# Kernel tuning notes

Hardware: AMD Instinct MI355X
Metric: run time of the kernel (lower is better)

The kernel has to match this reference:

```python
import jax, jax.numpy as jnp
import numpy as np

N, F_DIM, H, K, T = 4096, 256, 256, 3, 5
START, END = 10, 3  # args.len_numerical_features, args.num_class


def setup_inputs() -> dict:
    key = jax.random.key(0)
    ks = jax.random.split(key, 8)
    s = 0.05
    x = jax.random.normal(ks[0], (N, F_DIM), dtype=jnp.float32)
    adj = jax.random.randint(ks[1], (N, N, K), 0, 2, dtype=jnp.int32)
    gnn_w = jax.random.normal(ks[2], (K, F_DIM, H), dtype=jnp.float32) * s
    gnn_b = jnp.zeros((K, H), dtype=jnp.float32)
    w_ih = jax.random.normal(ks[3], (K, 4 * H, H), dtype=jnp.float32) * s
    w_hh = jax.random.normal(ks[4], (K, 4 * H, H), dtype=jnp.float32) * s
    b_ih = jnp.zeros((K, 4 * H), dtype=jnp.float32)
    b_hh = jnp.zeros((K, 4 * H), dtype=jnp.float32)
    fc_w = jax.random.normal(ks[5], (K, F_DIM, H), dtype=jnp.float32) * s
    fc_b = jnp.zeros((K, F_DIM), dtype=jnp.float32)
    return dict(x=x, gnn_w=gnn_w, gnn_b=gnn_b, w_ih=w_ih, w_hh=w_hh,
                b_ih=b_ih, b_hh=b_hh, fc_w=fc_w, fc_b=fc_b, adj=adj)


def _gcn(x, a_bin, w, b):
    # PyG GCNConv: A_hat = A + I (self-loops added on top of existing edges,
    # weight 1), out = D^-1/2 A_hat D^-1/2 (x @ W) + b
    a = a_bin + jnp.eye(N, dtype=x.dtype)
    deg = a.sum(axis=1)
    dinv = jnp.where(deg > 0, jax.lax.rsqrt(deg), 0.0)
    a_norm = dinv[:, None] * a * dinv[None, :]
    return a_norm @ (x @ w) + b


def _lstm_last(xt, w_ih, w_hh, b_ih, b_hh):
    # batch_first LSTM over T identical inputs xt [N,H]; returns h at last step
    def step(carry, _):
        h, c = carry
        g = xt @ w_ih.T + b_ih + h @ w_hh.T + b_hh
        i, f, gg, o = jnp.split(g, 4, axis=-1)  # torch gate order: i, f, g, o
        c = jax.nn.sigmoid(f) * c + jax.nn.sigmoid(i) * jnp.tanh(gg)
        h = jax.nn.sigmoid(o) * jnp.tanh(c)
        return (h, c), None
    zero = jnp.zeros((xt.shape[0], H), dtype=xt.dtype)
    (h, c), _ = jax.lax.scan(step, (zero, zero), None, length=T)
    return h


def _sig_slice(z):
    return z.at[:, START:F_DIM - END].set(jax.nn.sigmoid(z[:, START:F_DIM - END]))


def reference(x, gnn_w, gnn_b, w_ih, w_hh, b_ih, b_hh, fc_w, fc_b, adj):
    deltas, zbars = [], []
    for k in range(K):
        a_bin = (adj[:, :, k] != 0).astype(x.dtype)
        # GCN output is identical across timesteps -> compute once
        gnn_out = _gcn(x, a_bin, gnn_w[k], gnn_b[k])
        h_last = _lstm_last(gnn_out, w_ih[k], w_hh[k], b_ih[k], b_hh[k])
        delta = jnp.tanh(h_last @ fc_w[k].T + fc_b[k])  # [N, F]
        deltas.append(delta)
        zbars.append(_sig_slice(x + delta))
    delta_z = jnp.stack(deltas, -1).mean(-1)
    res_z_bar = jnp.stack(zbars, -1)  # [N, F, K]
    pred_matrix = _sig_slice(x + delta_z)
    return pred_matrix, res_z_bar, adj
```

## Files before the change

kernel.cpp:

```cpp
#include <hip/hip_runtime.h>
#include <stdint.h>

#define NN_ 4096
#define FD 256
#define HD 256
#define KC 3
#define GD 1024
#define SA 40
#define BPITCH 144

typedef __attribute__((ext_vector_type(4))) unsigned int vu4;
typedef __attribute__((ext_vector_type(4))) int vi4;
typedef __attribute__((ext_vector_type(4))) float vf4;
typedef __attribute__((ext_vector_type(4))) unsigned short vus4;
typedef __attribute__((ext_vector_type(8))) short short8;
typedef __attribute__((ext_vector_type(4))) float f32x4;

typedef __attribute__((address_space(1))) const void GV;
typedef __attribute__((address_space(3))) void LV;
__device__ __forceinline__ void gl16(const void* g, void* l) {
    __builtin_amdgcn_global_load_lds((GV*)g, (LV*)l, 16, 0, 0);
}

__device__ __forceinline__ float b2f(unsigned short u) {
    unsigned int v = ((unsigned int)u) << 16; float f; __builtin_memcpy(&f, &v, 4); return f;
}
__device__ __forceinline__ unsigned short f2b(float x) {
    unsigned int u; __builtin_memcpy(&u, &x, 4);
    u = (u + 0x7FFFu + ((u >> 16) & 1u)) >> 16;
    return (unsigned short)u;
}
__device__ __forceinline__ void cvt8(const float* __restrict__ g, unsigned short* o) {
    vf4 a = *(const vf4*)g, b = *(const vf4*)(g + 4);
    o[0] = f2b(a[0]); o[1] = f2b(a[1]); o[2] = f2b(a[2]); o[3] = f2b(a[3]);
    o[4] = f2b(b[0]); o[5] = f2b(b[1]); o[6] = f2b(b[2]); o[7] = f2b(b[3]);
}
__device__ __forceinline__ float frcp(float x) { return __builtin_amdgcn_rcpf(x); }
__device__ __forceinline__ float sigm(float v) { return frcp(1.f + __expf(-v)); }
__device__ __forceinline__ float ftanh(float v) { return 1.f - 2.f * frcp(__expf(2.f * v) + 1.f); }

__global__ __launch_bounds__(256) void adjxw(const int* __restrict__ adj,
        float* __restrict__ adj_out, unsigned char* __restrict__ abits,
        float* __restrict__ dinv, unsigned short* __restrict__ dinvb,
        const float* __restrict__ wih, const float* __restrict__ whh,
        const float* __restrict__ fcw, unsigned short* __restrict__ wb,
        const float* __restrict__ gnnw, const float* __restrict__ x,
        unsigned short* __restrict__ uT) {
    const int bid = blockIdx.x, t = threadIdx.x;
    __shared__ __align__(16) unsigned short sA[64 * SA], sB[64 * SA];
    __shared__ unsigned char nib[3][1024];
    __shared__ float r0[256], r1[256], r2[256];
    if (bid >= 4096) {
        const int b2 = bid - 4096;
        const int k = b2 >> 8, rem = b2 & 255, bn = rem >> 2, bg = rem & 3;
        const int lane = t & 63, wave = t >> 6;
        const int m = lane & 15, q = lane >> 4, ko = q * 8;
        const int h0 = bg * 64;
        f32x4 acc[4] = {};
        const float* A0 = x + (size_t)(bn * 64) * FD;
        const float* B0 = gnnw + (size_t)k * FD * HD;
        const int r = t >> 2, c8 = (t & 3) << 3;
        const int fB = t >> 3, c8B = (t & 7) << 3;
        for (int k0 = 0; k0 < FD; k0 += 32) {
            alignas(16) unsigned short tA[8], tB[8];
            cvt8(A0 + (size_t)r * FD + k0 + c8, tA);
            *(vu4*)(sA + r * SA + c8) = *(vu4*)tA;
            cvt8(B0 + (size_t)(k0 + fB) * HD + h0 + c8B, tB);
#pragma unroll
            for (int e = 0; e < 8; ++e) sB[(c8B + e) * SA + fB] = tB[e];
            __syncthreads();
            short8 af = *(const short8*)(sA + (wave * 16 + m) * SA + ko);
#pragma unroll
            for (int ct = 0; ct < 4; ++ct) {
                short8 bf = *(const short8*)(sB + (ct * 16 + m) * SA + ko);
                acc[ct] = __builtin_amdgcn_mfma_f32_16x16x32_bf16(af, bf, acc[ct], 0, 0, 0);
            }
            __syncthreads();
        }
        unsigned short* uTk = uT + (size_t)k * HD * NN_;
#pragma unroll
        for (int ct = 0; ct < 4; ++ct)
#pragma unroll
            for (int r2 = 0; r2 < 4; ++r2) {
                int col = h0 + ct * 16 + m;
                int row = bn * 64 + wave * 16 + q * 4 + r2;
                uTk[(size_t)col * NN_ + row] = f2b(acc[ct][r2]);
            }
        return;
    }
    const int i = bid;
    if (i < 864) {
        size_t e = ((size_t)i * 256 + t) * 8;
        const float* src; size_t off;
        if (e < 786432)       { src = wih; off = e; }
        else if (e < 1572864) { src = whh; off = e - 786432; }
        else                  { src = fcw; off = e - 1572864; }
        alignas(16) unsigned short o[8];
        cvt8(src + off, o);
        *(vu4*)(wb + e) = *(vu4*)o;
    }
    const int* src = adj + (size_t)i * 12288;
    float* dstf = adj_out + (size_t)i * 12288;
    float s0 = 0.f, s1 = 0.f, s2 = 0.f;
#pragma unroll
    for (int it = 0; it < 4; ++it) {
        int p = it * 256 + t;
        int jq = p * 4;
        vi4 a = *(const vi4*)(src + jq * 3);
        vi4 b = *(const vi4*)(src + jq * 3 + 4);
        vi4 c = *(const vi4*)(src + jq * 3 + 8);
        int vv[12] = {a[0],a[1],a[2],a[3],b[0],b[1],b[2],b[3],c[0],c[1],c[2],c[3]};
        float ff[12];
#pragma unroll
        for (int e = 0; e < 12; ++e) ff[e] = vv[e] ? 1.f : 0.f;
        vf4 w0 = {ff[0],ff[1],ff[2],ff[3]}, w1 = {ff[4],ff[5],ff[6],ff[7]}, w2 = {ff[8],ff[9],ff[10],ff[11]};
        *(vf4*)(dstf + jq * 3) = w0; *(vf4*)(dstf + jq * 3 + 4) = w1; *(vf4*)(dstf + jq * 3 + 8) = w2;
#pragma unroll
        for (int k = 0; k < 3; ++k) {
            unsigned int nb = (vv[k] ? 1u : 0u) | (vv[3 + k] ? 2u : 0u)
                            | (vv[6 + k] ? 4u : 0u) | (vv[9 + k] ? 8u : 0u);
            nib[k][p] = (unsigned char)nb;
        }
        s0 += ff[0] + ff[3] + ff[6] + ff[9];
        s1 += ff[1] + ff[4] + ff[7] + ff[10];
        s2 += ff[2] + ff[5] + ff[8] + ff[11];
    }
    r0[t] = s0; r1[t] = s1; r2[t] = s2;
    __syncthreads();
#pragma unroll
    for (int k = 0; k < 3; ++k) {
        unsigned int b0 = (unsigned int)nib[k][t * 4 + 0] | ((unsigned int)nib[k][t * 4 + 1] << 4);
        unsigned int b1 = (unsigned int)nib[k][t * 4 + 2] | ((unsigned int)nib[k][t * 4 + 3] << 4);
        *(unsigned short*)(abits + ((size_t)k * NN_ + i) * 512 + t * 2) =
            (unsigned short)(b0 | (b1 << 8));
    }
    for (int off = 128; off > 0; off >>= 1) {
        if (t < off) { r0[t] += r0[t + off]; r1[t] += r1[t + off]; r2[t] += r2[t + off]; }
        __syncthreads();
    }
    if (t == 0) {
        float d0 = 1.f / sqrtf(1.f + r0[0]);
        float d1 = 1.f / sqrtf(1.f + r1[0]);
        float d2 = 1.f / sqrtf(1.f + r2[0]);
        dinv[i]           = d0; dinvb[i]            = f2b(d0);
        dinv[NN_ + i]     = d1; dinvb[NN_ + i]      = f2b(d1);
        dinv[2 * NN_ + i] = d2; dinvb[2 * NN_ + i]  = f2b(d2);
    }
}

__global__ __launch_bounds__(256) void gemm_agg(const unsigned char* __restrict__ abits,
        const unsigned short* __restrict__ uT, const unsigned short* __restrict__ dinvb,
        const float* __restrict__ dinv, unsigned short* __restrict__ pbuf) {
    __shared__ __align__(16) unsigned char bitsA[128 * BPITCH];
    __shared__ __align__(16) unsigned short sB0[128 * 32];
    __shared__ __align__(16) unsigned short sB1[128 * 32];
    __shared__ __align__(16) unsigned short sDv[1024];
    const int d = blockIdx.x;
    const int w = (d & 7) * 96 + (d >> 3);
    const int bh = w & 1, bi = (w >> 1) & 31, z = w >> 6;
    const int k = z >> 2, s = z & 3;
    const int t = threadIdx.x, lane = t & 63, wave = t >> 6;
    const int wi = wave & 1, wh = wave >> 1;
    const int m = lane & 15, q = lane >> 4, ko = q * 8;
    const int i0 = bi * 128, h0 = bh * 128, jbase = s * 1024;
    {
        const int row = t >> 1, half = t & 1;
        const unsigned char* bsrc = abits + ((size_t)k * NN_ + i0 + row) * 512 + s * 128 + half * 64;
        unsigned char* bdst = bitsA + row * BPITCH + half * 64;
        vu4 v0 = *(const vu4*)(bsrc);
        vu4 v1 = *(const vu4*)(bsrc + 16);
        vu4 v2 = *(const vu4*)(bsrc + 32);
        vu4 v3 = *(const vu4*)(bsrc + 48);
        *(vu4*)(bdst)      = v0;
        *(vu4*)(bdst + 16) = v1;
        *(vu4*)(bdst + 32) = v2;
        *(vu4*)(bdst + 48) = v3;
    }
    if (t < 128)
        *(vu4*)(sDv + t * 8) = *(const vu4*)(dinvb + (size_t)k * NN_ + jbase + t * 8);
    f32x4 acc[4][4] = {};
    const int lrow = lane >> 2, lcol = (lane & 3) << 3;
    const unsigned short* Bg0 = uT + ((size_t)(k * 256 + h0 + wave * 32 + lrow)) * NN_ + jbase + lcol;
    const unsigned short* Bg1 = Bg0 + (size_t)16 * NN_;
    unsigned short* lB00 = sB0 + (wave * 32) * 32;
    unsigned short* lB01 = lB00 + 16 * 32;
    unsigned short* lB10 = sB1 + (wave * 32) * 32;
    unsigned short* lB11 = lB10 + 16 * 32;
    const int arowb = (wi * 64 + m) * BPITCH + q;
    for (int j0 = 0; j0 < 1024; j0 += 64) {
        gl16(Bg0 + j0, lB00);
        gl16(Bg1 + j0, lB01);
        gl16(Bg0 + j0 + 32, lB10);
        gl16(Bg1 + j0 + 32, lB11);
        __syncthreads();
        const int jby = j0 >> 3;
        short8 dv0 = *(const short8*)(sDv + j0 + ko);
        short8 dv1 = *(const short8*)(sDv + j0 + 32 + ko);
        short8 af0[4], af1[4];
#pragma unroll
        for (int rt = 0; rt < 4; ++rt) {
            unsigned int by0 = bitsA[arowb + rt * 16 * BPITCH + jby];
            unsigned int by1 = bitsA[arowb + rt * 16 * BPITCH + jby + 4];
#pragma unroll
            for (int e = 0; e < 8; ++e) {
                af0[rt][e] = (short)(((by0 >> e) & 1u) ? dv0[e] : (short)0);
                af1[rt][e] = (short)(((by1 >> e) & 1u) ? dv1[e] : (short)0);
            }
        }
#pragma unroll
        for (int ct = 0; ct < 4; ++ct) {
            short8 bf0 = *(const short8*)(sB0 + (wh * 64 + ct * 16 + m) * 32 + ko);
#pragma unroll
            for (int rt = 0; rt < 4; ++rt)
                acc[rt][ct] = __builtin_amdgcn_mfma_f32_16x16x32_bf16(af0[rt], bf0, acc[rt][ct], 0, 0, 0);
        }
#pragma unroll
        for (int ct = 0; ct < 4; ++ct) {
            short8 bf1 = *(const short8*)(sB1 + (wh * 64 + ct * 16 + m) * 32 + ko);
#pragma unroll
            for (int rt = 0; rt < 4; ++rt)
                acc[rt][ct] = __builtin_amdgcn_mfma_f32_16x16x32_bf16(af1[rt], bf1, acc[rt][ct], 0, 0, 0);
        }
        __syncthreads();
    }
    const int addself = ((bi >> 3) == s);
#pragma unroll
    for (int rt = 0; rt < 4; ++rt)
#pragma unroll
        for (int ct = 0; ct < 4; ++ct)
#pragma unroll
            for (int r2 = 0; r2 < 4; ++r2) {
                int row = i0 + wi * 64 + rt * 16 + q * 4 + r2;
                int col = h0 + wh * 64 + ct * 16 + m;
                float v = acc[rt][ct][r2];
                if (addself)
                    v += dinv[(size_t)k * NN_ + row]
                       * b2f(uT[((size_t)k * 256 + col) * NN_ + row]);
                pbuf[(((size_t)s * 3 + k) * NN_ + row) * 256 + col] = f2b(v);
            }
}

__global__ __launch_bounds__(256) void agg_reduce(const unsigned short* __restrict__ pbuf,
        const float* __restrict__ dinv, const float* __restrict__ gnnb,
        unsigned short* __restrict__ xt) {
    size_t e8 = ((size_t)blockIdx.x * 256 + threadIdx.x) * 8;
    int k = (int)(e8 >> 20);
    int i = (int)((e8 >> 8) & 4095);
    int h = (int)(e8 & 255);
    float di = dinv[k * NN_ + i];
    const size_t KIH = (size_t)KC * NN_ * HD;
    alignas(16) unsigned short p0[8], p1[8], p2[8], p3[8], o[8];
    *(vu4*)p0 = *(const vu4*)(pbuf + 0 * KIH + e8);
    *(vu4*)p1 = *(const vu4*)(pbuf + 1 * KIH + e8);
    *(vu4*)p2 = *(const vu4*)(pbuf + 2 * KIH + e8);
    *(vu4*)p3 = *(const vu4*)(pbuf + 3 * KIH + e8);
#pragma unroll
    for (int e = 0; e < 8; ++e) {
        float v = b2f(p0[e]) + b2f(p1[e]) + b2f(p2[e]) + b2f(p3[e]);
        o[e] = f2b(di * v + gnnb[k * HD + h + e]);
    }
    *(vu4*)(xt + e8) = *(vu4*)o;
}

__global__ __launch_bounds__(256) void lstm_gate(const unsigned short* __restrict__ A,
        const unsigned short* __restrict__ W, const float* __restrict__ b1,
        const float* __restrict__ b2, unsigned short* __restrict__ gX2,
        float* __restrict__ cbuf, unsigned short* __restrict__ hbuf) {
    __shared__ __align__(16) unsigned short sA0[128 * 32], sA1[128 * 32];
    __shared__ __align__(16) unsigned short sB0[128 * 32], sB1[128 * 32];
    const int d = blockIdx.x;
    const int w = (d & 7) * 96 + (d >> 3);
    const int chb = w & 7, bn = w >> 3;
    const int t = threadIdx.x, lane = t & 63, wave = t >> 6;
    const int m = lane & 15, q = lane >> 4, ko = q * 8;
    const int kk = bn >> 5;
    f32x4 acc[2][2][4] = {};
    const int lrow = lane >> 2, lcol = (lane & 3) << 3;
    const unsigned short* A0 = A + (size_t)bn * 128 * 256;
    const unsigned short* W0 = W + (size_t)kk * GD * 256 + (size_t)chb * 32 * 256;
    const unsigned short* Ag0 = A0 + (size_t)(wave * 32 + lrow) * 256 + lcol;
    const unsigned short* Ag1 = Ag0 + 16 * 256;
    const unsigned short* Bg0 = W0 + (size_t)(wave * 256 + lrow) * 256 + lcol;
    const unsigned short* Bg1 = Bg0 + 16 * 256;
    unsigned short* lA00 = sA0 + (wave * 32) * 32; unsigned short* lA01 = lA00 + 16 * 32;
    unsigned short* lA10 = sA1 + (wave * 32) * 32; unsigned short* lA11 = lA10 + 16 * 32;
    unsigned short* lB00 = sB0 + (wave * 32) * 32; unsigned short* lB01 = lB00 + 16 * 32;
    unsigned short* lB10 = sB1 + (wave * 32) * 32; unsigned short* lB11 = lB10 + 16 * 32;
    for (int k0 = 0; k0 < 256; k0 += 64) {
        gl16(Ag0 + k0, lA00);      gl16(Ag1 + k0, lA01);
        gl16(Ag0 + k0 + 32, lA10); gl16(Ag1 + k0 + 32, lA11);
        gl16(Bg0 + k0, lB00);      gl16(Bg1 + k0, lB01);
        gl16(Bg0 + k0 + 32, lB10); gl16(Bg1 + k0 + 32, lB11);
        __syncthreads();
        short8 af0[2], af1[2];
#pragma unroll
        for (int rt = 0; rt < 2; ++rt) {
            af0[rt] = *(const short8*)(sA0 + (wave * 32 + rt * 16 + m) * 32 + ko);
            af1[rt] = *(const short8*)(sA1 + (wave * 32 + rt * 16 + m) * 32 + ko);
        }
#pragma unroll
        for (int g = 0; g < 4; ++g)
#pragma unroll
            for (int cc = 0; cc < 2; ++cc) {
                short8 bf0 = *(const short8*)(sB0 + (g * 32 + cc * 16 + m) * 32 + ko);
#pragma unroll
                for (int rt = 0; rt < 2; ++rt)
                    acc[rt][cc][g] = __builtin_amdgcn_mfma_f32_16x16x32_bf16(af0[rt], bf0, acc[rt][cc][g], 0, 0, 0);
                short8 bf1 = *(const short8*)(sB1 + (g * 32 + cc * 16 + m) * 32 + ko);
#pragma unroll
                for (int rt = 0; rt < 2; ++rt)
                    acc[rt][cc][g] = __builtin_amdgcn_mfma_f32_16x16x32_bf16(af1[rt], bf1, acc[rt][cc][g], 0, 0, 0);
            }
        __syncthreads();
    }
#pragma unroll
    for (int rt = 0; rt < 2; ++rt)
#pragma unroll
        for (int cc = 0; cc < 2; ++cc)
#pragma unroll
            for (int r2 = 0; r2 < 4; ++r2) {
                int row = bn * 128 + wave * 32 + rt * 16 + q * 4 + r2;
                int ch = chb * 32 + cc * 16 + m;
                size_t goff = ((size_t)row * 256 + ch) * 4;
                size_t coff = (size_t)row * 256 + ch;
                float v[4];
                vus4 o;
#pragma unroll
                for (int g = 0; g < 4; ++g) {
                    v[g] = acc[rt][cc][g][r2]
                         + b1[kk * GD + g * 256 + ch] + b2[kk * GD + g * 256 + ch];
                    o[g] = f2b(v[g]);
                }
                *(vus4*)(gX2 + goff) = o;
                float cn = sigm(v[0]) * ftanh(v[2]);
                cbuf[coff] = cn;
                hbuf[coff] = f2b(sigm(v[3]) * ftanh(cn));
            }
}

__global__ __launch_bounds__(256) void lstm_step(const unsigned short* __restrict__ A,
        const unsigned short* __restrict__ W, const unsigned short* __restrict__ gX2,
        float* __restrict__ cbuf, unsigned short* __restrict__ hbuf) {
    __shared__ __align__(16) unsigned short sA0[128 * 32], sA1[128 * 32];
    __shared__ __align__(16) unsigned short sB0[128 * 32], sB1[128 * 32];
    const int d = blockIdx.x;
    const int w = (d & 7) * 96 + (d >> 3);
    const int chb = w & 7, bn = w >> 3;
    const int t = threadIdx.x, lane = t & 63, wave = t >> 6;
    const int m = lane & 15, q = lane >> 4, ko = q * 8;
    const int kk = bn >> 5;
    f32x4 acc[2][2][4] = {};
    const int lrow = lane >> 2, lcol = (lane & 3) << 3;
    const unsigned short* A0 = A + (size_t)bn * 128 * 256;
    const unsigned short* W0 = W + (size_t)kk * GD * 256 + (size_t)chb * 32 * 256;
    const unsigned short* Ag0 = A0 + (size_t)(wave * 32 + lrow) * 256 + lcol;
    const unsigned short* Ag1 = Ag0 + 16 * 256;
    const unsigned short* Bg0 = W0 + (size_t)(wave * 256 + lrow) * 256 + lcol;
    const unsigned short* Bg1 = Bg0 + 16 * 256;
    unsigned short* lA00 = sA0 + (wave * 32) * 32; unsigned short* lA01 = lA00 + 16 * 32;
    unsigned short* lA10 = sA1 + (wave * 32) * 32; unsigned short* lA11 = lA10 + 16 * 32;
    unsigned short* lB00 = sB0 + (wave * 32) * 32; unsigned short* lB01 = lB00 + 16 * 32;
    unsigned short* lB10 = sB1 + (wave * 32) * 32; unsigned short* lB11 = lB10 + 16 * 32;
    for (int k0 = 0; k0 < 256; k0 += 64) {
        gl16(Ag0 + k0, lA00);      gl16(Ag1 + k0, lA01);
        gl16(Ag0 + k0 + 32, lA10); gl16(Ag1 + k0 + 32, lA11);
        gl16(Bg0 + k0, lB00);      gl16(Bg1 + k0, lB01);
        gl16(Bg0 + k0 + 32, lB10); gl16(Bg1 + k0 + 32, lB11);
        __syncthreads();
        short8 af0[2], af1[2];
#pragma unroll
        for (int rt = 0; rt < 2; ++rt) {
            af0[rt] = *(const short8*)(sA0 + (wave * 32 + rt * 16 + m) * 32 + ko);
            af1[rt] = *(const short8*)(sA1 + (wave * 32 + rt * 16 + m) * 32 + ko);
        }
#pragma unroll
        for (int g = 0; g < 4; ++g)
#pragma unroll
            for (int cc = 0; cc < 2; ++cc) {
                short8 bf0 = *(const short8*)(sB0 + (g * 32 + cc * 16 + m) * 32 + ko);
#pragma unroll
                for (int rt = 0; rt < 2; ++rt)
                    acc[rt][cc][g] = __builtin_amdgcn_mfma_f32_16x16x32_bf16(af0[rt], bf0, acc[rt][cc][g], 0, 0, 0);
                short8 bf1 = *(const short8*)(sB1 + (g * 32 + cc * 16 + m) * 32 + ko);
#pragma unroll
                for (int rt = 0; rt < 2; ++rt)
                    acc[rt][cc][g] = __builtin_amdgcn_mfma_f32_16x16x32_bf16(af1[rt], bf1, acc[rt][cc][g], 0, 0, 0);
            }
        __syncthreads();
    }
#pragma unroll
    for (int rt = 0; rt < 2; ++rt)
#pragma unroll
        for (int cc = 0; cc < 2; ++cc)
#pragma unroll
            for (int r2 = 0; r2 < 4; ++r2) {
                int row = bn * 128 + wave * 32 + rt * 16 + q * 4 + r2;
                int ch = chb * 32 + cc * 16 + m;
                size_t goff = ((size_t)row * 256 + ch) * 4;
                size_t coff = (size_t)row * 256 + ch;
                vus4 gv = *(const vus4*)(gX2 + goff);
                float iv = acc[rt][cc][0][r2] + b2f(gv[0]);
                float fv = acc[rt][cc][1][r2] + b2f(gv[1]);
                float gg = acc[rt][cc][2][r2] + b2f(gv[2]);
                float ov = acc[rt][cc][3][r2] + b2f(gv[3]);
                float cn = sigm(fv) * cbuf[coff] + sigm(iv) * ftanh(gg);
                cbuf[coff] = cn;
                hbuf[coff] = f2b(sigm(ov) * ftanh(cn));
            }
}

__global__ __launch_bounds__(256) void fc_final(const unsigned short* __restrict__ A,
        const unsigned short* __restrict__ W, const float* __restrict__ fcb,
        const float* __restrict__ x, float* __restrict__ pred, float* __restrict__ res) {
    __shared__ __align__(16) unsigned short sA[3][64 * 32], sB[3][64 * 32];
    const int bg = blockIdx.x, bn = blockIdx.y;
    const int t = threadIdx.x, lane = t & 63, wave = t >> 6;
    const int m = lane & 15, q = lane >> 4, ko = q * 8;
    f32x4 acc[3][4] = {};
    const int lrow = lane >> 2, lcol = (lane & 3) << 3;
    const unsigned short* Ag[3]; const unsigned short* Bg[3];
#pragma unroll
    for (int k = 0; k < 3; ++k) {
        Ag[k] = A + ((size_t)k * NN_ + bn * 64 + wave * 16 + lrow) * HD + lcol;
        Bg[k] = W + ((size_t)k * FD + bg * 64 + wave * 16 + lrow) * HD + lcol;
    }
    for (int k0 = 0; k0 < HD; k0 += 32) {
#pragma unroll
        for (int k = 0; k < 3; ++k) {
            gl16(Ag[k] + k0, sA[k] + (wave * 16) * 32);
            gl16(Bg[k] + k0, sB[k] + (wave * 16) * 32);
        }
        __syncthreads();
#pragma unroll
        for (int k = 0; k < 3; ++k) {
            short8 af = *(const short8*)(sA[k] + (wave * 16 + m) * 32 + ko);
#pragma unroll
            for (int ct = 0; ct < 4; ++ct) {
                short8 bf = *(const short8*)(sB[k] + (ct * 16 + m) * 32 + ko);
                acc[k][ct] = __builtin_amdgcn_mfma_f32_16x16x32_bf16(af, bf, acc[k][ct], 0, 0, 0);
            }
        }
        __syncthreads();
    }
#pragma unroll
    for (int ct = 0; ct < 4; ++ct)
#pragma unroll
        for (int r2 = 0; r2 < 4; ++r2) {
            int col = bg * 64 + ct * 16 + m;
            int row = bn * 64 + wave * 16 + q * 4 + r2;
            float d0 = ftanh(acc[0][ct][r2] + fcb[col]);
            float d1 = ftanh(acc[1][ct][r2] + fcb[FD + col]);
            float d2 = ftanh(acc[2][ct][r2] + fcb[2 * FD + col]);
            float xf = x[(size_t)row * FD + col];
            bool sg = (col >= 10) && (col < 253);
            float dm = (d0 + d1 + d2) * (1.f / 3.f);
            float p = xf + dm; if (sg) p = sigm(p);
            pred[(size_t)row * FD + col] = p;
            float z0 = xf + d0; if (sg) z0 = sigm(z0);
            float z1 = xf + d1; if (sg) z1 = sigm(z1);
            float z2 = xf + d2; if (sg) z2 = sigm(z2);
            size_t rb = ((size_t)row * FD + col) * 3;
            res[rb] = z0; res[rb + 1] = z1; res[rb + 2] = z2;
        }
}

extern "C" void kernel_launch(void* const* d_in, const int* in_sizes, int n_in,
                              void* d_out, int out_size, void* d_ws, size_t ws_size,
                              hipStream_t stream) {
    const float* x    = (const float*)d_in[0];
    const float* gnnw = (const float*)d_in[1];
    const float* gnnb = (const float*)d_in[2];
    const float* wih  = (const float*)d_in[3];
    const float* whh  = (const float*)d_in[4];
    const float* bih  = (const float*)d_in[5];
    const float* bhh  = (const float*)d_in[6];
    const float* fcw  = (const float*)d_in[7];
    const float* fcb  = (const float*)d_in[8];
    const int*   adj  = (const int*)d_in[9];

    float* out = (float*)d_out;
    float* out_pred = out;
    float* out_res  = out + (size_t)NN_ * FD;
    float* out_adj  = out + (size_t)NN_ * FD * 4;

    char* ws = (char*)d_ws;
    float*          dinv  = (float*)ws;
    unsigned short* dinvb = (unsigned short*)(ws + 49152);
    unsigned short* R1    = (unsigned short*)(ws + 73728);
    unsigned short* H1    = (unsigned short*)(ws + 6365184);
    unsigned short* XT    = (unsigned short*)(ws + 12656640);
    unsigned short* wb    = (unsigned short*)(ws + 18948096);
    unsigned char*  abits = (unsigned char*)(ws + 22487040);
    unsigned short* pbuf  = (unsigned short*)(ws + 28778496);
    unsigned short* gX2   = (unsigned short*)(ws + 53944320);
    float*          cbuf  = (float*)(ws + 79110144);
    const unsigned short* wihb = wb;
    const unsigned short* whhb = wb + 786432;
    const unsigned short* fcwb = wb + 1572864;
    (void)ws_size; (void)in_sizes; (void)n_in; (void)out_size;

    adjxw<<<dim3(4864), 256, 0, stream>>>(adj, out_adj, abits, dinv, dinvb,
                                          wih, whh, fcw, wb, gnnw, x, R1 );
    gemm_agg<<<dim3(768), 256, 0, stream>>>(abits, R1 , dinvb, dinv, pbuf);
    agg_reduce<<<dim3(1536), 256, 0, stream>>>(pbuf, dinv, gnnb, XT);
    lstm_gate<<<dim3(768), 256, 0, stream>>>(XT, wihb, bih, bhh, gX2, cbuf, R1);
    lstm_step<<<dim3(768), 256, 0, stream>>>(R1, whhb, gX2, cbuf, H1);
    lstm_step<<<dim3(768), 256, 0, stream>>>(H1, whhb, gX2, cbuf, R1);
    lstm_step<<<dim3(768), 256, 0, stream>>>(R1, whhb, gX2, cbuf, H1);
    lstm_step<<<dim3(768), 256, 0, stream>>>(H1, whhb, gX2, cbuf, R1);
    fc_final<<<dim3(4, 64), 256, 0, stream>>>(R1, fcwb, fcb, x, out_pred, out_res);
}
```

Before: 572.6 us.

## Remap LSTM GEMM waves to a 2x2 grid and add row-major U copy

The LSTM gate and step kernels change how the four waves split the 128x32-channel tile. Each wave now covers 64 rows by 16 channels instead of 32 rows by 32 channels, so it loads 4 A fragments and 1 B fragment per gate. This cuts redundant B-fragment LDS reads while using the same 16 accumulators. Separately, adjxw also writes a row-major copy of x@W, so the self-loop epilogue in gemm_agg reads contiguous columns instead of a strided transposed buffer. The cost is an extra workspace buffer and extra global writes.

```diff
diff --git a/kernel.cpp b/kernel.cpp
--- a/kernel.cpp
+++ b/kernel.cpp
@@ -45,7 +45,7 @@
         const float* __restrict__ wih, const float* __restrict__ whh,
         const float* __restrict__ fcw, unsigned short* __restrict__ wb,
         const float* __restrict__ gnnw, const float* __restrict__ x,
-        unsigned short* __restrict__ uT) {
+        unsigned short* __restrict__ uT, unsigned short* __restrict__ u2) {
     const int bid = blockIdx.x, t = threadIdx.x;
     __shared__ __align__(16) unsigned short sA[64 * SA], sB[64 * SA];
     __shared__ unsigned char nib[3][1024];
@@ -78,13 +78,16 @@
             __syncthreads();
         }
         unsigned short* uTk = uT + (size_t)k * HD * NN_;
+        unsigned short* u2k = u2 + (size_t)k * NN_ * HD;
 #pragma unroll
         for (int ct = 0; ct < 4; ++ct)
 #pragma unroll
             for (int r2 = 0; r2 < 4; ++r2) {
                 int col = h0 + ct * 16 + m;
                 int row = bn * 64 + wave * 16 + q * 4 + r2;
-                uTk[(size_t)col * NN_ + row] = f2b(acc[ct][r2]);
+                unsigned short uv = f2b(acc[ct][r2]);
+                uTk[(size_t)col * NN_ + row] = uv;
+                u2k[(size_t)row * HD + col] = uv;
             }
         return;
     }
@@ -149,8 +152,9 @@
 }
 
 __global__ __launch_bounds__(256) void gemm_agg(const unsigned char* __restrict__ abits,
-        const unsigned short* __restrict__ uT, const unsigned short* __restrict__ dinvb,
-        const float* __restrict__ dinv, unsigned short* __restrict__ pbuf) {
+        const unsigned short* __restrict__ uT, const unsigned short* __restrict__ u2,
+        const unsigned short* __restrict__ dinvb, const float* __restrict__ dinv,
+        unsigned short* __restrict__ pbuf) {
     __shared__ __align__(16) unsigned char bitsA[128 * BPITCH];
     __shared__ __align__(16) unsigned short sB0[128 * 32];
     __shared__ __align__(16) unsigned short sB1[128 * 32];
@@ -235,7 +239,7 @@
                 float v = acc[rt][ct][r2];
                 if (addself)
                     v += dinv[(size_t)k * NN_ + row]
-                       * b2f(uT[((size_t)k * 256 + col) * NN_ + row]);
+                       * b2f(u2[((size_t)k * NN_ + row) * HD + col]);
                 pbuf[(((size_t)s * 3 + k) * NN_ + row) * 256 + col] = f2b(v);
             }
 }
@@ -272,9 +276,10 @@
     const int w = (d & 7) * 96 + (d >> 3);
     const int chb = w & 7, bn = w >> 3;
     const int t = threadIdx.x, lane = t & 63, wave = t >> 6;
+    const int wr = wave & 1, wch = wave >> 1;
     const int m = lane & 15, q = lane >> 4, ko = q * 8;
     const int kk = bn >> 5;
-    f32x4 acc[2][2][4] = {};
+    f32x4 acc[4][4] = {};
     const int lrow = lane >> 2, lcol = (lane & 3) << 3;
     const unsigned short* A0 = A + (size_t)bn * 128 * 256;
     const unsigned short* W0 = W + (size_t)kk * GD * 256 + (size_t)chb * 32 * 256;
@@ -292,50 +297,46 @@
         gl16(Bg0 + k0, lB00);      gl16(Bg1 + k0, lB01);
         gl16(Bg0 + k0 + 32, lB10); gl16(Bg1 + k0 + 32, lB11);
         __syncthreads();
-        short8 af0[2], af1[2];
-#pragma unroll
-        for (int rt = 0; rt < 2; ++rt) {
-            af0[rt] = *(const short8*)(sA0 + (wave * 32 + rt * 16 + m) * 32 + ko);
-            af1[rt] = *(const short8*)(sA1 + (wave * 32 + rt * 16 + m) * 32 + ko);
-        }
-#pragma unroll
-        for (int g = 0; g < 4; ++g)
-#pragma unroll
-            for (int cc = 0; cc < 2; ++cc) {
-                short8 bf0 = *(const short8*)(sB0 + (g * 32 + cc * 16 + m) * 32 + ko);
-#pragma unroll
-                for (int rt = 0; rt < 2; ++rt)
-                    acc[rt][cc][g] = __builtin_amdgcn_mfma_f32_16x16x32_bf16(af0[rt], bf0, acc[rt][cc][g], 0, 0, 0);
-                short8 bf1 = *(const short8*)(sB1 + (g * 32 + cc * 16 + m) * 32 + ko);
-#pragma unroll
-                for (int rt = 0; rt < 2; ++rt)
-                    acc[rt][cc][g] = __builtin_amdgcn_mfma_f32_16x16x32_bf16(af1[rt], bf1, acc[rt][cc][g], 0, 0, 0);
+        short8 af0[4], af1[4];
+#pragma unroll
+        for (int rt = 0; rt < 4; ++rt) {
+            af0[rt] = *(const short8*)(sA0 + (wr * 64 + rt * 16 + m) * 32 + ko);
+            af1[rt] = *(const short8*)(sA1 + (wr * 64 + rt * 16 + m) * 32 + ko);
+        }
+#pragma unroll
+        for (int g = 0; g < 4; ++g) {
+            short8 bf0 = *(const short8*)(sB0 + (g * 32 + wch * 16 + m) * 32 + ko);
+#pragma unroll
+            for (int rt = 0; rt < 4; ++rt)
+                acc[rt][g] = __builtin_amdgcn_mfma_f32_16x16x32_bf16(af0[rt], bf0, acc[rt][g], 0, 0, 0);
+            short8 bf1 = *(const short8*)(sB1 + (g * 32 + wch * 16 + m) * 32 + ko);
+#pragma unroll
+            for (int rt = 0; rt < 4; ++rt)
+                acc[rt][g] = __builtin_amdgcn_mfma_f32_16x16x32_bf16(af1[rt], bf1, acc[rt][g], 0, 0, 0);
+        }
+        __syncthreads();
+    }
+#pragma unroll
+    for (int rt = 0; rt < 4; ++rt)
+#pragma unroll
+        for (int r2 = 0; r2 < 4; ++r2) {
+            int row = bn * 128 + wr * 64 + rt * 16 + q * 4 + r2;
+            int ch = chb * 32 + wch * 16 + m;
+            size_t goff = ((size_t)row * 256 + ch) * 4;
+            size_t coff = (size_t)row * 256 + ch;
+            float v[4];
+            vus4 o;
+#pragma unroll
+            for (int g = 0; g < 4; ++g) {
+                v[g] = acc[rt][g][r2]
+                     + b1[kk * GD + g * 256 + ch] + b2[kk * GD + g * 256 + ch];
+                o[g] = f2b(v[g]);
             }
-        __syncthreads();
-    }
-#pragma unroll
-    for (int rt = 0; rt < 2; ++rt)
-#pragma unroll
-        for (int cc = 0; cc < 2; ++cc)
-#pragma unroll
-            for (int r2 = 0; r2 < 4; ++r2) {
-                int row = bn * 128 + wave * 32 + rt * 16 + q * 4 + r2;
-                int ch = chb * 32 + cc * 16 + m;
-                size_t goff = ((size_t)row * 256 + ch) * 4;
-                size_t coff = (size_t)row * 256 + ch;
-                float v[4];
-                vus4 o;
-#pragma unroll
-                for (int g = 0; g < 4; ++g) {
-                    v[g] = acc[rt][cc][g][r2]
-                         + b1[kk * GD + g * 256 + ch] + b2[kk * GD + g * 256 + ch];
-                    o[g] = f2b(v[g]);
-                }
-                *(vus4*)(gX2 + goff) = o;
-                float cn = sigm(v[0]) * ftanh(v[2]);
-                cbuf[coff] = cn;
-                hbuf[coff] = f2b(sigm(v[3]) * ftanh(cn));
-            }
+            *(vus4*)(gX2 + goff) = o;
+            float cn = sigm(v[0]) * ftanh(v[2]);
+            cbuf[coff] = cn;
+            hbuf[coff] = f2b(sigm(v[3]) * ftanh(cn));
+        }
 }
 
 __global__ __launch_bounds__(256) void lstm_step(const unsigned short* __restrict__ A,
@@ -347,9 +348,10 @@
     const int w = (d & 7) * 96 + (d >> 3);
     const int chb = w & 7, bn = w >> 3;
     const int t = threadIdx.x, lane = t & 63, wave = t >> 6;
+    const int wr = wave & 1, wch = wave >> 1;
     const int m = lane & 15, q = lane >> 4, ko = q * 8;
     const int kk = bn >> 5;
-    f32x4 acc[2][2][4] = {};
+    f32x4 acc[4][4] = {};
     const int lrow = lane >> 2, lcol = (lane & 3) << 3;
     const unsigned short* A0 = A + (size_t)bn * 128 * 256;
     const unsigned short* W0 = W + (size_t)kk * GD * 256 + (size_t)chb * 32 * 256;
@@ -367,46 +369,42 @@
         gl16(Bg0 + k0, lB00);      gl16(Bg1 + k0, lB01);
         gl16(Bg0 + k0 + 32, lB10); gl16(Bg1 + k0 + 32, lB11);
         __syncthreads();
-        short8 af0[2], af1[2];
-#pragma unroll
-        for (int rt = 0; rt < 2; ++rt) {
-            af0[rt] = *(const short8*)(sA0 + (wave * 32 + rt * 16 + m) * 32 + ko);
-            af1[rt] = *(const short8*)(sA1 + (wave * 32 + rt * 16 + m) * 32 + ko);
-        }
-#pragma unroll
-        for (int g = 0; g < 4; ++g)
-#pragma unroll
-            for (int cc = 0; cc < 2; ++cc) {
-                short8 bf0 = *(const short8*)(sB0 + (g * 32 + cc * 16 + m) * 32 + ko);
-#pragma unroll
-                for (int rt = 0; rt < 2; ++rt)
-                    acc[rt][cc][g] = __builtin_amdgcn_mfma_f32_16x16x32_bf16(af0[rt], bf0, acc[rt][cc][g], 0, 0, 0);
-                short8 bf1 = *(const short8*)(sB1 + (g * 32 + cc * 16 + m) * 32 + ko);
-#pragma unroll
-                for (int rt = 0; rt < 2; ++rt)
-                    acc[rt][cc][g] = __builtin_amdgcn_mfma_f32_16x16x32_bf16(af1[rt], bf1, acc[rt][cc][g], 0, 0, 0);
-            }
-        __syncthreads();
-    }
-#pragma unroll
-    for (int rt = 0; rt < 2; ++rt)
-#pragma unroll
-        for (int cc = 0; cc < 2; ++cc)
-#pragma unroll
-            for (int r2 = 0; r2 < 4; ++r2) {
-                int row = bn * 128 + wave * 32 + rt * 16 + q * 4 + r2;
-                int ch = chb * 32 + cc * 16 + m;
-                size_t goff = ((size_t)row * 256 + ch) * 4;
-                size_t coff = (size_t)row * 256 + ch;
-                vus4 gv = *(const vus4*)(gX2 + goff);
-                float iv = acc[rt][cc][0][r2] + b2f(gv[0]);
-                float fv = acc[rt][cc][1][r2] + b2f(gv[1]);
-                float gg = acc[rt][cc][2][r2] + b2f(gv[2]);
-                float ov = acc[rt][cc][3][r2] + b2f(gv[3]);
-                float cn = sigm(fv) * cbuf[coff] + sigm(iv) * ftanh(gg);
-                cbuf[coff] = cn;
-                hbuf[coff] = f2b(sigm(ov) * ftanh(cn));
-            }
+        short8 af0[4], af1[4];
+#pragma unroll
+        for (int rt = 0; rt < 4; ++rt) {
+            af0[rt] = *(const short8*)(sA0 + (wr * 64 + rt * 16 + m) * 32 + ko);
+            af1[rt] = *(const short8*)(sA1 + (wr * 64 + rt * 16 + m) * 32 + ko);
+        }
+#pragma unroll
+        for (int g = 0; g < 4; ++g) {
+            short8 bf0 = *(const short8*)(sB0 + (g * 32 + wch * 16 + m) * 32 + ko);
+#pragma unroll
+            for (int rt = 0; rt < 4; ++rt)
+                acc[rt][g] = __builtin_amdgcn_mfma_f32_16x16x32_bf16(af0[rt], bf0, acc[rt][g], 0, 0, 0);
+            short8 bf1 = *(const short8*)(sB1 + (g * 32 + wch * 16 + m) * 32 + ko);
+#pragma unroll
+            for (int rt = 0; rt < 4; ++rt)
+                acc[rt][g] = __builtin_amdgcn_mfma_f32_16x16x32_bf16(af1[rt], bf1, acc[rt][g], 0, 0, 0);
+        }
+        __syncthreads();
+    }
+#pragma unroll
+    for (int rt = 0; rt < 4; ++rt)
+#pragma unroll
+        for (int r2 = 0; r2 < 4; ++r2) {
+            int row = bn * 128 + wr * 64 + rt * 16 + q * 4 + r2;
+            int ch = chb * 32 + wch * 16 + m;
+            size_t goff = ((size_t)row * 256 + ch) * 4;
+            size_t coff = (size_t)row * 256 + ch;
+            vus4 gv = *(const vus4*)(gX2 + goff);
+            float iv = acc[rt][0][r2] + b2f(gv[0]);
+            float fv = acc[rt][1][r2] + b2f(gv[1]);
+            float gg = acc[rt][2][r2] + b2f(gv[2]);
+            float ov = acc[rt][3][r2] + b2f(gv[3]);
+            float cn = sigm(fv) * cbuf[coff] + sigm(iv) * ftanh(gg);
+            cbuf[coff] = cn;
+            hbuf[coff] = f2b(sigm(ov) * ftanh(cn));
+        }
 }
 
 __global__ __launch_bounds__(256) void fc_final(const unsigned short* __restrict__ A,
@@ -494,14 +492,15 @@
     unsigned short* pbuf  = (unsigned short*)(ws + 28778496);
     unsigned short* gX2   = (unsigned short*)(ws + 53944320);
     float*          cbuf  = (float*)(ws + 79110144);
+    unsigned short* U2    = (unsigned short*)(ws + 91693056);
     const unsigned short* wihb = wb;
     const unsigned short* whhb = wb + 786432;
     const unsigned short* fcwb = wb + 1572864;
     (void)ws_size; (void)in_sizes; (void)n_in; (void)out_size;
 
     adjxw<<<dim3(4864), 256, 0, stream>>>(adj, out_adj, abits, dinv, dinvb,
-                                          wih, whh, fcw, wb, gnnw, x, R1 );
-    gemm_agg<<<dim3(768), 256, 0, stream>>>(abits, R1 , dinvb, dinv, pbuf);
+                                          wih, whh, fcw, wb, gnnw, x, R1 , U2);
+    gemm_agg<<<dim3(768), 256, 0, stream>>>(abits, R1 , U2, dinvb, dinv, pbuf);
     agg_reduce<<<dim3(1536), 256, 0, stream>>>(pbuf, dinv, gnnb, XT);
     lstm_gate<<<dim3(768), 256, 0, stream>>>(XT, wihb, bih, bhh, gX2, cbuf, R1);
     lstm_step<<<dim3(768), 256, 0, stream>>>(R1, whhb, gX2, cbuf, H1);
```

Measured after the change: 577.4 us. No clear change (+0.8%).
